# Kernel tuning notes

Measured on AMD Instinct MI355X. Metric: run time of the kernel, lower is better.

## Reference

```python
import jax, jax.numpy as jnp
import numpy as np

DIM = 384
HEADS = 12
WIN = (7, 7)
N = WIN[0] * WIN[1]
B = 4096
NW = 64  # number of windows sharing one mask


def _relative_position_index(win):
    wh, ww = win
    coords = np.stack(np.meshgrid(np.arange(wh), np.arange(ww), indexing='ij'))  # (2,wh,ww)
    flat = coords.reshape(2, -1)                                                 # (2, N)
    rel = flat[:, :, None] - flat[:, None, :]                                    # (2, N, N)
    rel = rel.transpose(1, 2, 0).astype(np.int64)
    rel[:, :, 0] += wh - 1
    rel[:, :, 1] += ww - 1
    rel[:, :, 0] *= 2 * ww - 1
    return jnp.asarray(rel.sum(-1), dtype=jnp.int32)                             # (N, N)


def setup_inputs() -> dict:
    key = jax.random.key(0)
    ks = jax.random.split(key, 7)
    std = 0.02
    return {
        'x': jax.random.normal(ks[0], (B, N, DIM), jnp.float32),
        'mask': jax.random.normal(ks[1], (NW, N, N), jnp.float32),
        'qkv_w': jax.random.normal(ks[2], (3 * DIM, DIM), jnp.float32) * std,
        'qkv_b': jnp.zeros((3 * DIM,), jnp.float32),
        'bias_table': jax.random.normal(ks[3], ((2 * WIN[0] - 1) * (2 * WIN[1] - 1), HEADS), jnp.float32) * std,
        'proj_w': jax.random.normal(ks[4], (DIM, DIM), jnp.float32) * std,
        'proj_b': jnp.zeros((DIM,), jnp.float32),
        'rel_idx': _relative_position_index(WIN),
    }


def reference(x, mask, qkv_w, qkv_b, bias_table, proj_w, proj_b, rel_idx):
    B_, n, c = x.shape
    h = HEADS
    d = c // h
    scale = d ** -0.5

    qkv = x @ qkv_w.T + qkv_b                                  # (B_, N, 3C)
    qkv = qkv.reshape(B_, n, 3, h, d).transpose(2, 0, 3, 1, 4)  # (3, B_, H, N, D)
    q, k, v = qkv[0], qkv[1], qkv[2]

    attn = jnp.einsum('bhnd,bhmd->bhnm', q, k) * scale          # (B_, H, N, N)

    bias = bias_table[rel_idx]                                  # (N, N, H)
    attn = attn + bias.transpose(2, 0, 1)[None]                 # add (1, H, N, N)

    nW = mask.shape[0]
    attn = attn.reshape(B_ // nW, nW, h, n, n) + mask[None, :, None]
    attn = attn.reshape(B_, h, n, n)

    attn = jax.nn.softmax(attn, axis=-1)
    out = jnp.einsum('bhnm,bhmd->bhnd', attn, v)                # (B_, H, N, D)
    out = out.transpose(0, 2, 1, 3).reshape(B_, n, c)
    return out @ proj_w.T + proj_b
```

## Files before the change

### kernel.cpp

```cpp
#include <hip/hip_runtime.h>

typedef __bf16 bf16;
typedef __bf16 bf16x4 __attribute__((ext_vector_type(4)));
typedef __bf16 bf16x8 __attribute__((ext_vector_type(8)));
typedef float f32x4 __attribute__((ext_vector_type(4)));
typedef float f32x16 __attribute__((ext_vector_type(16)));
typedef int i32x2 __attribute__((ext_vector_type(2)));
typedef unsigned int u32;

#define DIMC 384
#define NHEADS 12
#define NTOK 49
#define NWINB 4096
#define MROWS (NWINB*NTOK)

#define MFMA32(A,B,C) __builtin_amdgcn_mfma_f32_32x32x16_bf16(A,B,C,0,0,0)

#define GLOAD16(gsrc, lbase) \
  __builtin_amdgcn_global_load_lds( \
      (const __attribute__((address_space(1))) u32*)(gsrc), \
      (__attribute__((address_space(3))) u32*)(lbase), 16, 0, 0)

__global__ __launch_bounds__(256) void k_convert(const float4* __restrict__ in,
                                                 bf16x4* __restrict__ out, int n4) {
  int stride = gridDim.x * blockDim.x;
  for (int i = blockIdx.x * blockDim.x + threadIdx.x; i < n4; i += stride) {
    float4 v = in[i];
    bf16x4 o;
    o[0] = (bf16)v.x; o[1] = (bf16)v.y; o[2] = (bf16)v.z; o[3] = (bf16)v.w;
    out[i] = o;
  }
}

__global__ __launch_bounds__(256) void k_biasT(const float* __restrict__ table,
                                               const int* __restrict__ rel,
                                               float* __restrict__ outp) {
  int i = blockIdx.x * 256 + threadIdx.x;
  if (i < NHEADS * NTOK * NTOK) {
    int h = i / (NTOK * NTOK), r2 = i - h * (NTOK * NTOK);
    int key = r2 / NTOK, q = r2 - key * NTOK;
    outp[i] = table[rel[q * NTOK + key] * NHEADS + h];
  }
}

__global__ __launch_bounds__(256) void k_maskT(const float* __restrict__ mask,
                                               float* __restrict__ outp) {
  int i = blockIdx.x * 256 + threadIdx.x;
  if (i < 64 * NTOK * NTOK) {
    int w = i / (NTOK * NTOK), r2 = i - w * (NTOK * NTOK);
    int key = r2 / NTOK, q = r2 - key * NTOK;
    outp[i] = mask[(w * NTOK + q) * NTOK + key];
  }
}

template <int MODE>
__global__ __launch_bounds__(256) void k_gemm(const bf16* __restrict__ A,
                                              const bf16* __restrict__ Bw,
                                              const float* __restrict__ bias,
                                              bf16* __restrict__ oQ, bf16* __restrict__ oK,
                                              bf16* __restrict__ oV, float* __restrict__ oP) {
  __shared__ __align__(16) bf16 lA[128 * 64];
  __shared__ __align__(16) bf16 lB[128 * 64];
  const int t = threadIdx.x;
  const int l = t & 63;
  const int wv = t >> 6;
  const int wr = wv >> 1, wc = wv & 1;

  const u32 NXB = MODE == 0 ? 9 : 3;
  const u32 nwg = NXB * (MROWS / 128);
  u32 lin = blockIdx.y * gridDim.x + blockIdx.x;
  u32 logical = (lin & 7) * (nwg >> 3) + (lin >> 3);
  const int n0 = (int)(logical % NXB) * 128;
  const int m0 = (int)(logical / NXB) * 128;

  const int lr = l & 15, lg = l >> 4;

  const int srow = wv * 32 + (l >> 3);
  const int scolb = (l & 7) * 16;

  f32x4 acc[4][4] = {};

  for (int k0 = 0; k0 < DIMC; k0 += 64) {
    __syncthreads();
#pragma unroll
    for (int i = 0; i < 4; ++i) {
      int row = srow + i * 8;
      int scol = (scolb ^ ((row & 7) << 4)) >> 1;
      GLOAD16(&A[(size_t)(m0 + row) * DIMC + k0 + scol], &lA[wv * 2048 + i * 512]);
      GLOAD16(&Bw[(size_t)(n0 + row) * DIMC + k0 + scol], &lB[wv * 2048 + i * 512]);
    }
    __syncthreads();
#pragma unroll
    for (int kk = 0; kk < 64; kk += 32) {
      bf16x8 af[4], bfv[4];
#pragma unroll
      for (int f = 0; f < 4; ++f) {
        int row = wr * 64 + f * 16 + lr;
        int cb = (kk + lg * 8) * 2;
        af[f] = *reinterpret_cast<const bf16x8*>(
            &lA[row * 64 + ((cb ^ ((row & 7) << 4)) >> 1)]);
      }
#pragma unroll
      for (int f = 0; f < 4; ++f) {
        int row = wc * 64 + f * 16 + lr;
        int cb = (kk + lg * 8) * 2;
        bfv[f] = *reinterpret_cast<const bf16x8*>(
            &lB[row * 64 + ((cb ^ ((row & 7) << 4)) >> 1)]);
      }
#pragma unroll
      for (int fm = 0; fm < 4; ++fm)
#pragma unroll
        for (int fn = 0; fn < 4; ++fn)
          acc[fm][fn] = __builtin_amdgcn_mfma_f32_16x16x32_bf16(af[fm], bfv[fn], acc[fm][fn], 0, 0, 0);
    }
  }

#pragma unroll
  for (int fm = 0; fm < 4; ++fm) {
#pragma unroll
    for (int fn = 0; fn < 4; ++fn) {
      int c = n0 + wc * 64 + fn * 16 + lr;
      float bc = bias[c];
#pragma unroll
      for (int r = 0; r < 4; ++r) {
        int m = m0 + wr * 64 + fm * 16 + lg * 4 + r;
        float v = acc[fm][fn][r] + bc;
        if (MODE == 0) {
          int b = m / 49, n = m - b * 49;
          int which = c / 384;
          int rem = c - which * 384;
          int h = rem >> 5, d = rem & 31;
          bf16* dst = which == 0 ? oQ : (which == 1 ? oK : oV);
          dst[((b * 12 + h) * 49 + n) * 32 + d] = (bf16)v;
        } else {
          oP[m * 384 + c] = v;
        }
      }
    }
  }
}

__global__ __launch_bounds__(256, 4) void k_attn(const bf16* __restrict__ Q,
                                                 const bf16* __restrict__ K,
                                                 const bf16* __restrict__ V,
                                                 const float* __restrict__ biasT,
                                                 const float* __restrict__ maskT,
                                                 bf16* __restrict__ H) {
  __shared__ __align__(16) bf16 Vl[4][32 * 72];
  const int t = threadIdx.x, l = t & 63, wv = t >> 6;
  const int p = blockIdx.x * 4 + wv;
  const int b = p / 12, h = p - b * 12;
  const int w = b & 63;
  const size_t base = (size_t)p * (49 * 32);
  const int c = l & 31, b5 = l >> 5;
  bf16* vl = Vl[wv];

  {
    bf16x4 z = {};
    for (int i = l; i < 128; i += 64) {
      int d = i >> 2, kq = 48 + (i & 3) * 4;
      *reinterpret_cast<bf16x4*>(&vl[d * 72 + kq]) = z;
    }
  }
  for (int i = l; i < 392; i += 64) {
    int key = i >> 3, dc = (i & 7) * 4;
    bf16x4 vv = *reinterpret_cast<const bf16x4*>(&V[base + key * 32 + dc]);
#pragma unroll
    for (int j = 0; j < 4; ++j) vl[(dc + j) * 72 + key] = vv[j];
  }

  bf16x8 kf[2][2], qf[2][2];
#pragma unroll
  for (int f = 0; f < 2; ++f) {
    int row = f * 32 + c; if (row > 48) row = 48;
#pragma unroll
    for (int kd = 0; kd < 2; ++kd) {
      kf[f][kd] = *reinterpret_cast<const bf16x8*>(&K[base + row * 32 + kd * 16 + b5 * 8]);
      qf[f][kd] = *reinterpret_cast<const bf16x8*>(&Q[base + row * 32 + kd * 16 + b5 * 8]);
    }
  }

  const float scale = 0.17677669529663689f;
  const float* bT = biasT + h * 2401;
  const float* mT = maskT + w * 2401;

#pragma unroll
  for (int fn = 0; fn < 2; ++fn) {
    f32x16 s0 = {}, s1 = {};
    s0 = MFMA32(kf[0][0], qf[fn][0], s0);
    s0 = MFMA32(kf[0][1], qf[fn][1], s0);
    s1 = MFMA32(kf[1][0], qf[fn][0], s1);
    s1 = MFMA32(kf[1][1], qf[fn][1], s1);

    int q = fn * 32 + c;
    int qc = q > 48 ? 48 : q;

    float vals[32];
    float vmax = -1e30f;
#pragma unroll
    for (int fm = 0; fm < 2; ++fm) {
#pragma unroll
      for (int r = 0; r < 16; ++r) {
        int key = fm * 32 + (r & 3) + 8 * (r >> 2) + 4 * b5;
        float sv = fm ? s1[r] : s0[r];
        float v;
        if (key < 49) {
          float cm = bT[key * 49 + qc] + mT[key * 49 + qc];
          v = fmaf(sv, scale, cm);
        } else {
          v = -1e30f;
        }
        vals[fm * 16 + r] = v;
        vmax = fmaxf(vmax, v);
      }
    }
    vmax = fmaxf(vmax, __shfl_xor(vmax, 32));
    float sum = 0.f;
#pragma unroll
    for (int i = 0; i < 32; ++i) {
      float e = __expf(vals[i] - vmax);
      vals[i] = e;
      sum += e;
    }
    sum += __shfl_xor(sum, 32);
    float inv = 1.f / sum;

    f32x16 o = {};
#pragma unroll
    for (int kk = 0; kk < 4; ++kk) {
      int ib = (kk >> 1) * 16 + 8 * (kk & 1);
      union { bf16 hh[2]; u32 u; } cv;
      u32 A0, A1, B0, B1;
      cv.hh[0] = (bf16)(vals[ib + 0] * inv); cv.hh[1] = (bf16)(vals[ib + 1] * inv); A0 = cv.u;
      cv.hh[0] = (bf16)(vals[ib + 2] * inv); cv.hh[1] = (bf16)(vals[ib + 3] * inv); A1 = cv.u;
      cv.hh[0] = (bf16)(vals[ib + 4] * inv); cv.hh[1] = (bf16)(vals[ib + 5] * inv); B0 = cv.u;
      cv.hh[0] = (bf16)(vals[ib + 6] * inv); cv.hh[1] = (bf16)(vals[ib + 7] * inv); B1 = cv.u;
      i32x2 sw0 = __builtin_amdgcn_permlane32_swap((int)A0, (int)B0, false, false);
      i32x2 sw1 = __builtin_amdgcn_permlane32_swap((int)A1, (int)B1, false, false);
      union { u32 d[4]; bf16x8 v8; } pa;
      pa.d[0] = (u32)sw0[0]; pa.d[1] = (u32)sw1[0];
      pa.d[2] = (u32)sw0[1]; pa.d[3] = (u32)sw1[1];
      bf16x8 vf = *reinterpret_cast<const bf16x8*>(&vl[c * 72 + kk * 16 + b5 * 8]);
      o = MFMA32(pa.v8, vf, o);
    }

#pragma unroll
    for (int r = 0; r < 16; ++r) {
      int qrow = fn * 32 + (r & 3) + 8 * (r >> 2) + 4 * b5;
      if (qrow < 49)
        H[((size_t)b * 49 + qrow) * 384 + h * 32 + c] = (bf16)o[r];
    }
  }
}

extern "C" void kernel_launch(void* const* d_in, const int* in_sizes, int n_in,
                              void* d_out, int out_size, void* d_ws, size_t ws_size,
                              hipStream_t stream) {
  const float* x     = (const float*)d_in[0];
  const float* mask  = (const float*)d_in[1];
  const float* qkvw  = (const float*)d_in[2];
  const float* qkvb  = (const float*)d_in[3];
  const float* btab  = (const float*)d_in[4];
  const float* projw = (const float*)d_in[5];
  const float* projb = (const float*)d_in[6];
  const int*   rel   = (const int*)d_in[7];
  float* out = (float*)d_out;

  const size_t NELEM = (size_t)MROWS * DIMC;
  char* ws = (char*)d_ws;
  bf16*  xb    = (bf16*)ws;
  bf16*  vb    = (bf16*)(ws + 154140672);
  float* biasT = (float*)(ws + 308281344);
  bf16*  wqkv  = (bf16*)(ws + 308396800);
  float* maskT = (float*)(ws + 308396800);
  bf16*  wproj = (bf16*)(ws + 309281536);
  bf16* qb = (bf16*)d_out;
  bf16* kb = qb + NELEM;

  k_convert<<<2048, 256, 0, stream>>>((const float4*)x, (bf16x4*)xb, (int)(NELEM / 4));
  k_convert<<<432, 256, 0, stream>>>((const float4*)qkvw, (bf16x4*)wqkv, 3 * DIMC * DIMC / 4);
  k_convert<<<144, 256, 0, stream>>>((const float4*)projw, (bf16x4*)wproj, DIMC * DIMC / 4);
  k_biasT<<<(NHEADS * NTOK * NTOK + 255) / 256, 256, 0, stream>>>(btab, rel, biasT);

  k_gemm<0><<<dim3(1152 / 128, MROWS / 128), 256, 0, stream>>>(xb, wqkv, qkvb, qb, kb, vb, nullptr);
  k_maskT<<<(64 * NTOK * NTOK + 255) / 256, 256, 0, stream>>>(mask, maskT);
  k_attn<<<(NWINB * NHEADS) / 4, 256, 0, stream>>>(qb, kb, vb, biasT, maskT, xb);
  k_gemm<1><<<dim3(384 / 128, MROWS / 128), 256, 0, stream>>>(xb, wproj, projb, nullptr, nullptr, nullptr, out);
}
```

Measured before the change: 865.8 us.

## Double-buffer LDS tiles in GEMM to overlap global loads with MFMA

New measurement: 843.3 us. 1.03x faster.

```diff
diff --git a/kernel.cpp b/kernel.cpp
--- a/kernel.cpp
+++ b/kernel.cpp
@@ -59,8 +59,8 @@
                                               const float* __restrict__ bias,
                                               bf16* __restrict__ oQ, bf16* __restrict__ oK,
                                               bf16* __restrict__ oV, float* __restrict__ oP) {
-  __shared__ __align__(16) bf16 lA[128 * 64];
-  __shared__ __align__(16) bf16 lB[128 * 64];
+  __shared__ __align__(16) bf16 lA[2][128 * 64];
+  __shared__ __align__(16) bf16 lB[2][128 * 64];
   const int t = threadIdx.x;
   const int l = t & 63;
   const int wv = t >> 6;
@@ -80,16 +80,38 @@
 
   f32x4 acc[4][4] = {};
 
-  for (int k0 = 0; k0 < DIMC; k0 += 64) {
-    __syncthreads();
-#pragma unroll
-    for (int i = 0; i < 4; ++i) {
-      int row = srow + i * 8;
-      int scol = (scolb ^ ((row & 7) << 4)) >> 1;
-      GLOAD16(&A[(size_t)(m0 + row) * DIMC + k0 + scol], &lA[wv * 2048 + i * 512]);
-      GLOAD16(&Bw[(size_t)(n0 + row) * DIMC + k0 + scol], &lB[wv * 2048 + i * 512]);
-    }
-    __syncthreads();
+  int scolA[4];
+#pragma unroll
+  for (int i = 0; i < 4; ++i) {
+    int row = srow + i * 8;
+    scolA[i] = (scolb ^ ((row & 7) << 4)) >> 1;
+  }
+
+#define STAGE(BUF, K0)                                                            \
+  {                                                                               \
+    _Pragma("unroll") for (int i = 0; i < 4; ++i) {                               \
+      int row = srow + i * 8;                                                     \
+      GLOAD16(&A[(size_t)(m0 + row) * DIMC + (K0) + scolA[i]],                    \
+              &lA[BUF][wv * 2048 + i * 512]);                                     \
+      GLOAD16(&Bw[(size_t)(n0 + row) * DIMC + (K0) + scolA[i]],                   \
+              &lB[BUF][wv * 2048 + i * 512]);                                     \
+    }                                                                             \
+  }
+
+  STAGE(0, 0);
+
+#pragma unroll
+  for (int tt = 0; tt < 6; ++tt) {
+    const int cur = tt & 1;
+    if (tt > 0) __builtin_amdgcn_s_barrier();
+    if (tt < 5) {
+      STAGE(cur ^ 1, (tt + 1) * 64);
+      asm volatile("s_waitcnt vmcnt(8)" ::: "memory");
+    } else {
+      asm volatile("s_waitcnt vmcnt(0)" ::: "memory");
+    }
+    __builtin_amdgcn_s_barrier();
+
 #pragma unroll
     for (int kk = 0; kk < 64; kk += 32) {
       bf16x8 af[4], bfv[4];
@@ -98,14 +120,14 @@
         int row = wr * 64 + f * 16 + lr;
         int cb = (kk + lg * 8) * 2;
         af[f] = *reinterpret_cast<const bf16x8*>(
-            &lA[row * 64 + ((cb ^ ((row & 7) << 4)) >> 1)]);
+            &lA[cur][row * 64 + ((cb ^ ((row & 7) << 4)) >> 1)]);
       }
 #pragma unroll
       for (int f = 0; f < 4; ++f) {
         int row = wc * 64 + f * 16 + lr;
         int cb = (kk + lg * 8) * 2;
         bfv[f] = *reinterpret_cast<const bf16x8*>(
-            &lB[row * 64 + ((cb ^ ((row & 7) << 4)) >> 1)]);
+            &lB[cur][row * 64 + ((cb ^ ((row & 7) << 4)) >> 1)]);
       }
 #pragma unroll
       for (int fm = 0; fm < 4; ++fm)
@@ -114,6 +136,7 @@
           acc[fm][fn] = __builtin_amdgcn_mfma_f32_16x16x32_bf16(af[fm], bfv[fn], acc[fm][fn], 0, 0, 0);
     }
   }
+#undef STAGE
 
 #pragma unroll
   for (int fm = 0; fm < 4; ++fm) {
```
